# Kernel optimization log

Measured on AMD Instinct MI355X. Metric: run time of the kernel, lower is better.

Reference implementation:

```python
import jax, jax.numpy as jnp
import numpy as np
from jax import lax

B, H, W = 64, 64, 64
N_CHANNELS = 16
N_FILTERS = 128
N_DENSE = 256
T_STEPS = 60  # update_time() with Tmin=60, Tmax=61


def setup_inputs() -> dict:
    key = jax.random.key(0)
    ks = jax.random.split(key, 7)
    s_conv = 1.0 / np.sqrt(3 * 3 * N_CHANNELS)
    s_d1 = 1.0 / np.sqrt(N_FILTERS)
    s_d2 = 1.0 / np.sqrt(N_DENSE)
    return {
        "input": jax.random.uniform(ks[0], (B, H, W), dtype=jnp.float32),
        # conv kernel in HWIO layout for lax.conv_general_dilated
        "conv_w": jax.random.uniform(ks[1], (3, 3, N_CHANNELS, N_FILTERS), jnp.float32, -s_conv, s_conv),
        "conv_b": jax.random.uniform(ks[2], (N_FILTERS,), jnp.float32, -s_conv, s_conv),
        "w1": jax.random.uniform(ks[3], (N_FILTERS, N_DENSE), jnp.float32, -s_d1, s_d1),
        "b1": jax.random.uniform(ks[4], (N_DENSE,), jnp.float32, -s_d1, s_d1),
        "w2": jax.random.uniform(ks[5], (N_DENSE, N_CHANNELS), jnp.float32, -s_d2, s_d2),
        "b2": jax.random.uniform(ks[6], (N_CHANNELS,), jnp.float32, -s_d2, s_d2),
    }


def reference(input, conv_w, conv_b, w1, b1, w2, b2):
    # grid: (B,H,W,C), channel 0 seeded with the input image
    grid = jnp.zeros((B, H, W, N_CHANNELS), dtype=input.dtype)
    grid = grid.at[..., 0].set(input)
    # zero channel 0 of the delta (channel 0 is frozen)
    ch_mask = (jnp.arange(N_CHANNELS) != 0).astype(input.dtype)  # (C,)

    def step(g, _):
        conv = lax.conv_general_dilated(
            g, conv_w, window_strides=(1, 1), padding="SAME",
            dimension_numbers=("NHWC", "HWIO", "NHWC")) + conv_b
        h = jax.nn.relu(conv)                       # (B,H,W,F)
        d = jax.nn.relu(h @ w1 + b1) @ w2 + b2      # (B,H,W,C)
        alive = (g[..., 0:1] > 0.1).astype(g.dtype)  # (B,H,W,1)
        g = g + d * ch_mask * alive
        return g, None

    grid, _ = lax.scan(step, grid, None, length=T_STEPS)
    return jax.nn.softmax(grid[..., 1:11], axis=-1)  # (B,H,W,10)
```

## Files before the change

### kernel.cpp

```cpp
#include <hip/hip_runtime.h>
#include <math.h>

typedef _Float16 f16;
typedef f16  f16x8 __attribute__((ext_vector_type(8)));
typedef f16  f16x4 __attribute__((ext_vector_type(4)));
typedef float f32x4 __attribute__((ext_vector_type(4)));

#define NB 64
#define NC 16
#define NF 128
#define ND 256
#define NSTEP 60
#define GRID_ELEMS (NB*64*64*NC)
#define NPIX (NB*64*64)

#define KCONV 160
#define HSS   136
#define RPS   18

#define OFF_CW 0
#define OFF_W1 20480
#define OFF_W2 53248

__global__ void init_grid(const float* __restrict__ inp, float* __restrict__ g) {
    int i = blockIdx.x * 256 + threadIdx.x;
    if (i >= GRID_ELEMS) return;
    int c = i & 15;
    g[i] = (c == 0) ? inp[i >> 4] : 0.0f;
}

__global__ void prep_weights(const float* __restrict__ cw, const float* __restrict__ w1,
                             const float* __restrict__ w2, f16* __restrict__ wb) {
    int i = blockIdx.x * 256 + threadIdx.x;
    float v; int off, idx;
    if (i < 20480) {
        int f = i / 160, k = i - f * 160;
        v = (k < 144) ? cw[k * 128 + f] : 0.0f;
        off = OFF_CW; idx = i;
    } else if (i < 20480 + 32768) {
        int r = i - 20480;
        int j = r >> 7, f = r & 127;
        v = w1[f * 256 + j];
        off = OFF_W1; idx = r;
    } else {
        int r = i - 20480 - 32768;
        int c = r >> 8, j = r & 255;
        v = w2[j * 16 + c];
        off = OFF_W2; idx = r;
    }
    wb[off + idx] = (f16)v;
}

__global__ __launch_bounds__(256, 2) void nca_step(
    const float* __restrict__ gin, float* __restrict__ gout,
    const f16* __restrict__ wb,
    const float* __restrict__ cb, const float* __restrict__ b1, const float* __restrict__ b2)
{
    __shared__ f16 smem[40000];
    f16* const hs   = smem;
    f16* const halo = smem + 34816;
    float* const redF = (float*)smem;

    const int t    = threadIdx.x;
    const int w    = t >> 6;
    const int lane = t & 63;
    const int q    = lane >> 4;
    const int l16  = lane & 15;

    const int d  = blockIdx.x;
    const int b  = ((d & 7) << 3) | (d >> 7);
    const int tl = (d >> 3) & 15;
    const int y0 = (tl >> 2) << 4;
    const int x0 = (tl & 3) << 4;

    const float* gb  = gin  + (size_t)b * 64 * 64 * 16;
    float*       gob = gout + (size_t)b * 64 * 64 * 16;

    const int fbase = w << 5;
    f16x8 cA[2][5];
    #pragma unroll
    for (int ft = 0; ft < 2; ++ft)
        #pragma unroll
        for (int kc = 0; kc < 5; ++kc)
            cA[ft][kc] = *(const f16x8*)(wb + OFF_CW +
                (size_t)(fbase + ft * 16 + l16) * KCONV + kc * 32 + q * 8);

    for (int i = t; i < 1296; i += 256) {
        int c4 = (i & 3) << 2;
        int xy = i >> 2;
        int xx = xy % 18;
        int yy = xy / 18;
        int gy = y0 + yy - 1, gx = x0 + xx - 1;
        f32x4 v = {0.f, 0.f, 0.f, 0.f};
        if ((unsigned)gy < 64u && (unsigned)gx < 64u)
            v = *(const f32x4*)(gb + (gy * 64 + gx) * 16 + c4);
        f16x4 hv;
        hv.x = (f16)v.x; hv.y = (f16)v.y; hv.z = (f16)v.z; hv.w = (f16)v.w;
        *(f16x4*)(halo + xy * 16 + c4) = hv;
    }
    __syncthreads();

    for (int half = 0; half < 2; ++half) {
        f32x4 acc[2][8];
        #pragma unroll
        for (int ft = 0; ft < 2; ++ft) {
            f32x4 bias;
            bias.x = cb[fbase + ft * 16 + q * 4 + 0];
            bias.y = cb[fbase + ft * 16 + q * 4 + 1];
            bias.z = cb[fbase + ft * 16 + q * 4 + 2];
            bias.w = cb[fbase + ft * 16 + q * 4 + 3];
            #pragma unroll
            for (int p = 0; p < 8; ++p) acc[ft][p] = bias;
        }

        #pragma unroll
        for (int kc = 0; kc < 5; ++kc) {
            int tap = kc * 2 + (q >> 1);
            if (tap > 8) tap = 8;
            int dy = tap / 3, dx = tap - dy * 3;
            #pragma unroll
            for (int p = 0; p < 8; ++p) {
                int hy = half * 8 + p + dy;
                int hx = l16 + dx;
                f16x8 bf = *(const f16x8*)(halo + (hy * 18 + hx) * 16 + (q & 1) * 8);
                #pragma unroll
                for (int ft = 0; ft < 2; ++ft)
                    acc[ft][p] = __builtin_amdgcn_mfma_f32_16x16x32_f16(cA[ft][kc], bf, acc[ft][p], 0, 0, 0);
            }
        }

        #pragma unroll
        for (int ft = 0; ft < 2; ++ft)
            #pragma unroll
            for (int p = 0; p < 8; ++p) {
                f32x4 a = acc[ft][p];
                f16x4 pk;
                pk.x = (f16)fmaxf(a.x, 0.0f);
                pk.y = (f16)fmaxf(a.y, 0.0f);
                pk.z = (f16)fmaxf(a.z, 0.0f);
                pk.w = (f16)fmaxf(a.w, 0.0f);
                *(f16x4*)(hs + (half * 128 + p * 16 + l16) * HSS + fbase + ft * 16 + q * 4) = pk;
            }
    }
    __syncthreads();

    const int tyy = t >> 4, txx = t & 15;
    const size_t tpixb = ((size_t)(y0 + tyy) * 64 + (x0 + txx)) * 16;
    const float a0 = gb[tpixb];
    f32x4 gv4[4];
    #pragma unroll
    for (int h = 0; h < 4; ++h) gv4[h] = *(const f32x4*)(gb + tpixb + h * 4);

    const int jbase = w << 6;
    f16x8 dA[2][2][4];
    float b1v[2][2][4];
    #pragma unroll
    for (int jp = 0; jp < 2; ++jp)
        #pragma unroll
        for (int jt2 = 0; jt2 < 2; ++jt2) {
            #pragma unroll
            for (int kc = 0; kc < 4; ++kc)
                dA[jp][jt2][kc] = *(const f16x8*)(wb + OFF_W1 +
                    (size_t)(jbase + jp * 32 + jt2 * 16 + l16) * 128 + kc * 32 + q * 8);
            #pragma unroll
            for (int r = 0; r < 4; ++r)
                b1v[jp][jt2][r] = b1[jbase + jp * 32 + jt2 * 16 + q * 4 + r];
        }
    f16x4 w2k[4];
    #pragma unroll
    for (int jt = 0; jt < 4; ++jt)
        w2k[jt] = *(const f16x4*)(wb + OFF_W2 + (size_t)l16 * 256 + jbase + jt * 16 + q * 4);

    f32x4 dacc[16];
    #pragma unroll
    for (int p = 0; p < 16; ++p) { dacc[p].x = 0.f; dacc[p].y = 0.f; dacc[p].z = 0.f; dacc[p].w = 0.f; }

    for (int p = 0; p < 16; ++p) {
        f16x8 hB[4];
        #pragma unroll
        for (int kc = 0; kc < 4; ++kc)
            hB[kc] = *(const f16x8*)(hs + (p * 16 + l16) * HSS + kc * 32 + q * 8);

        #pragma unroll
        for (int jp = 0; jp < 2; ++jp)
            #pragma unroll
            for (int jt2 = 0; jt2 < 2; ++jt2) {
                f32x4 a1;
                a1.x = b1v[jp][jt2][0]; a1.y = b1v[jp][jt2][1];
                a1.z = b1v[jp][jt2][2]; a1.w = b1v[jp][jt2][3];
                #pragma unroll
                for (int kc = 0; kc < 4; ++kc)
                    a1 = __builtin_amdgcn_mfma_f32_16x16x32_f16(dA[jp][jt2][kc], hB[kc], a1, 0, 0, 0);
                f16x4 pk;
                pk.x = (f16)fmaxf(a1.x, 0.0f);
                pk.y = (f16)fmaxf(a1.y, 0.0f);
                pk.z = (f16)fmaxf(a1.z, 0.0f);
                pk.w = (f16)fmaxf(a1.w, 0.0f);
                dacc[p] = __builtin_amdgcn_mfma_f32_16x16x16f16(pk, w2k[jp * 2 + jt2], dacc[p], 0, 0, 0);
            }
    }

    __syncthreads();
    #pragma unroll
    for (int p = 0; p < 16; ++p)
        #pragma unroll
        for (int r = 0; r < 4; ++r) {
            int px = p * 16 + q * 4 + r;
            redF[(w * 256 + px) * RPS + l16] = dacc[p][r];
        }
    __syncthreads();

    {
        const int px = t;
        const bool alive = (a0 > 0.1f);
        #pragma unroll
        for (int h = 0; h < 4; ++h) {
            const int ch = h * 4;
            f32x4 v0 = *(const f32x4*)(redF + (0 * 256 + px) * RPS + ch);
            f32x4 v1 = *(const f32x4*)(redF + (1 * 256 + px) * RPS + ch);
            f32x4 v2 = *(const f32x4*)(redF + (2 * 256 + px) * RPS + ch);
            f32x4 v3 = *(const f32x4*)(redF + (3 * 256 + px) * RPS + ch);
            f32x4 sv = v0 + v1 + v2 + v3;
            f32x4 ov;
            #pragma unroll
            for (int i = 0; i < 4; ++i) {
                int c = ch + i;
                float nv = gv4[h][i];
                if (alive && c != 0) nv += sv[i] + b2[c];
                ov[i] = nv;
            }
            *(f32x4*)(gob + tpixb + ch) = ov;
        }
    }
}

__global__ void softmax_out(const float* __restrict__ g, float* __restrict__ out) {
    int pix = blockIdx.x * 256 + threadIdx.x;
    if (pix >= NPIX) return;
    const float* gp = g + (size_t)pix * 16;
    float v[10];
    float m = -1e30f;
    #pragma unroll
    for (int i = 0; i < 10; ++i) { v[i] = gp[1 + i]; m = fmaxf(m, v[i]); }
    float s = 0.f;
    #pragma unroll
    for (int i = 0; i < 10; ++i) { v[i] = __expf(v[i] - m); s += v[i]; }
    float inv = 1.0f / s;
    float* op = out + (size_t)pix * 10;
    #pragma unroll
    for (int i = 0; i < 10; ++i) op[i] = v[i] * inv;
}

extern "C" void kernel_launch(void* const* d_in, const int* in_sizes, int n_in,
                              void* d_out, int out_size, void* d_ws, size_t ws_size,
                              hipStream_t stream) {
    const float* inp = (const float*)d_in[0];
    const float* cw  = (const float*)d_in[1];
    const float* cb  = (const float*)d_in[2];
    const float* w1  = (const float*)d_in[3];
    const float* b1  = (const float*)d_in[4];
    const float* w2  = (const float*)d_in[5];
    const float* b2  = (const float*)d_in[6];
    float* out = (float*)d_out;

    float* g0 = (float*)d_ws;
    float* g1 = g0 + GRID_ELEMS;
    f16* wb = (f16*)d_out;

    prep_weights<<<224, 256, 0, stream>>>(cw, w1, w2, wb);
    init_grid<<<(GRID_ELEMS + 255) / 256, 256, 0, stream>>>(inp, g0);

    float* bufs[2] = { g0, g1 };
    for (int s = 0; s < NSTEP; ++s) {
        nca_step<<<1024, 256, 0, stream>>>(bufs[s & 1], bufs[(s + 1) & 1],
                                           wb, cb, b1, b2);
    }
    softmax_out<<<(NPIX + 255) / 256, 256, 0, stream>>>(g0, out);
}
```

Measured before the change: 2.499 ms.

## Partition dense MLP by pixel rows per wave instead of hidden units, drop LDS reduction

Each wave now owns 4 pixel rows of the tile and loops over all 256 hidden units, keeping the h activations in registers and streaming W1/W2 slices from global memory. Because every wave computes the full sum for its own pixels, the cross-wave LDS reduction and its two barriers are gone, and results are written straight to the output grid. In exchange, weights are reloaded from global/L2 on every hidden tile, not held in registers, and the output stores become scalar per-lane writes instead of vectorised ones.

```diff
diff --git a/kernel.cpp b/kernel.cpp
--- a/kernel.cpp
+++ b/kernel.cpp
@@ -16,7 +16,6 @@
 
 #define KCONV 160
 #define HSS   136
-#define RPS   18
 
 #define OFF_CW 0
 #define OFF_W1 20480
@@ -59,7 +58,6 @@
     __shared__ f16 smem[40000];
     f16* const hs   = smem;
     f16* const halo = smem + 34816;
-    float* const redF = (float*)smem;
 
     const int t    = threadIdx.x;
     const int w    = t >> 6;
@@ -144,92 +142,57 @@
     }
     __syncthreads();
 
-    const int tyy = t >> 4, txx = t & 15;
-    const size_t tpixb = ((size_t)(y0 + tyy) * 64 + (x0 + txx)) * 16;
-    const float a0 = gb[tpixb];
-    f32x4 gv4[4];
-    #pragma unroll
-    for (int h = 0; h < 4; ++h) gv4[h] = *(const f32x4*)(gb + tpixb + h * 4);
-
-    const int jbase = w << 6;
-    f16x8 dA[2][2][4];
-    float b1v[2][2][4];
-    #pragma unroll
-    for (int jp = 0; jp < 2; ++jp)
-        #pragma unroll
-        for (int jt2 = 0; jt2 < 2; ++jt2) {
+    const int pbase = w << 2;
+
+    f16x8 hB[4][4];
+    #pragma unroll
+    for (int pp = 0; pp < 4; ++pp)
+        #pragma unroll
+        for (int kc = 0; kc < 4; ++kc)
+            hB[pp][kc] = *(const f16x8*)(hs + ((pbase + pp) * 16 + l16) * HSS + kc * 32 + q * 8);
+
+    f32x4 dacc[4];
+    #pragma unroll
+    for (int pp = 0; pp < 4; ++pp) { dacc[pp].x = 0.f; dacc[pp].y = 0.f; dacc[pp].z = 0.f; dacc[pp].w = 0.f; }
+
+    #pragma unroll 1
+    for (int jt = 0; jt < 16; ++jt) {
+        f16x8 dAk[4];
+        #pragma unroll
+        for (int kc = 0; kc < 4; ++kc)
+            dAk[kc] = *(const f16x8*)(wb + OFF_W1 +
+                (size_t)(jt * 16 + l16) * 128 + kc * 32 + q * 8);
+        f32x4 b1v = *(const f32x4*)(b1 + jt * 16 + q * 4);
+        f16x4 w2f = *(const f16x4*)(wb + OFF_W2 + (size_t)l16 * 256 + jt * 16 + q * 4);
+
+        #pragma unroll
+        for (int pp = 0; pp < 4; ++pp) {
+            f32x4 a1 = b1v;
             #pragma unroll
             for (int kc = 0; kc < 4; ++kc)
-                dA[jp][jt2][kc] = *(const f16x8*)(wb + OFF_W1 +
-                    (size_t)(jbase + jp * 32 + jt2 * 16 + l16) * 128 + kc * 32 + q * 8);
-            #pragma unroll
-            for (int r = 0; r < 4; ++r)
-                b1v[jp][jt2][r] = b1[jbase + jp * 32 + jt2 * 16 + q * 4 + r];
-        }
-    f16x4 w2k[4];
-    #pragma unroll
-    for (int jt = 0; jt < 4; ++jt)
-        w2k[jt] = *(const f16x4*)(wb + OFF_W2 + (size_t)l16 * 256 + jbase + jt * 16 + q * 4);
-
-    f32x4 dacc[16];
-    #pragma unroll
-    for (int p = 0; p < 16; ++p) { dacc[p].x = 0.f; dacc[p].y = 0.f; dacc[p].z = 0.f; dacc[p].w = 0.f; }
-
-    for (int p = 0; p < 16; ++p) {
-        f16x8 hB[4];
-        #pragma unroll
-        for (int kc = 0; kc < 4; ++kc)
-            hB[kc] = *(const f16x8*)(hs + (p * 16 + l16) * HSS + kc * 32 + q * 8);
-
-        #pragma unroll
-        for (int jp = 0; jp < 2; ++jp)
-            #pragma unroll
-            for (int jt2 = 0; jt2 < 2; ++jt2) {
-                f32x4 a1;
-                a1.x = b1v[jp][jt2][0]; a1.y = b1v[jp][jt2][1];
-                a1.z = b1v[jp][jt2][2]; a1.w = b1v[jp][jt2][3];
-                #pragma unroll
-                for (int kc = 0; kc < 4; ++kc)
-                    a1 = __builtin_amdgcn_mfma_f32_16x16x32_f16(dA[jp][jt2][kc], hB[kc], a1, 0, 0, 0);
-                f16x4 pk;
-                pk.x = (f16)fmaxf(a1.x, 0.0f);
-                pk.y = (f16)fmaxf(a1.y, 0.0f);
-                pk.z = (f16)fmaxf(a1.z, 0.0f);
-                pk.w = (f16)fmaxf(a1.w, 0.0f);
-                dacc[p] = __builtin_amdgcn_mfma_f32_16x16x16f16(pk, w2k[jp * 2 + jt2], dacc[p], 0, 0, 0);
-            }
-    }
-
-    __syncthreads();
-    #pragma unroll
-    for (int p = 0; p < 16; ++p)
+                a1 = __builtin_amdgcn_mfma_f32_16x16x32_f16(dAk[kc], hB[pp][kc], a1, 0, 0, 0);
+            f16x4 pk;
+            pk.x = (f16)fmaxf(a1.x, 0.0f);
+            pk.y = (f16)fmaxf(a1.y, 0.0f);
+            pk.z = (f16)fmaxf(a1.z, 0.0f);
+            pk.w = (f16)fmaxf(a1.w, 0.0f);
+            dacc[pp] = __builtin_amdgcn_mfma_f32_16x16x16f16(pk, w2f, dacc[pp], 0, 0, 0);
+        }
+    }
+
+    const float b2v = b2[l16];
+    #pragma unroll
+    for (int pp = 0; pp < 4; ++pp) {
+        const int prow = pbase + pp;
         #pragma unroll
         for (int r = 0; r < 4; ++r) {
-            int px = p * 16 + q * 4 + r;
-            redF[(w * 256 + px) * RPS + l16] = dacc[p][r];
-        }
-    __syncthreads();
-
-    {
-        const int px = t;
-        const bool alive = (a0 > 0.1f);
-        #pragma unroll
-        for (int h = 0; h < 4; ++h) {
-            const int ch = h * 4;
-            f32x4 v0 = *(const f32x4*)(redF + (0 * 256 + px) * RPS + ch);
-            f32x4 v1 = *(const f32x4*)(redF + (1 * 256 + px) * RPS + ch);
-            f32x4 v2 = *(const f32x4*)(redF + (2 * 256 + px) * RPS + ch);
-            f32x4 v3 = *(const f32x4*)(redF + (3 * 256 + px) * RPS + ch);
-            f32x4 sv = v0 + v1 + v2 + v3;
-            f32x4 ov;
-            #pragma unroll
-            for (int i = 0; i < 4; ++i) {
-                int c = ch + i;
-                float nv = gv4[h][i];
-                if (alive && c != 0) nv += sv[i] + b2[c];
-                ov[i] = nv;
-            }
-            *(f32x4*)(gob + tpixb + ch) = ov;
+            const int px = prow * 16 + q * 4 + r;
+            const int yy = px >> 4, xx = px & 15;
+            const size_t pixb = ((size_t)(y0 + yy) * 64 + (x0 + xx)) * 16;
+            const float a0 = gb[pixb];
+            float nv = gb[pixb + l16];
+            if (a0 > 0.1f && l16 != 0) nv += dacc[pp][r] + b2v;
+            gob[pixb + l16] = nv;
         }
     }
 }
```

New measurement: 3.166 ms. 1.27x slower.

## Repartition waves 2x2 over pixels and filters, stream weights per k-chunk

Applied to the files above, without the earlier changes.

Changes the wave split from four waves each owning a slice of filters and dense units across all 256 pixels to a 2x2 split over pixel halves and filter/dense halves. Conv weights and W1 tiles are now streamed per k-chunk or j-tile with a one-step register prefetch instead of being held entirely in registers. The final cross-wave reduction drops from four partials to two, with the reduction buffer stride changed to 17. The aim is lower register pressure and less reduction traffic, at the cost of more global/L2 weight loads inside the loops and scalar rather than vector LDS reads in the reduction.

```diff
diff --git a/kernel.cpp b/kernel.cpp
--- a/kernel.cpp
+++ b/kernel.cpp
@@ -16,7 +16,7 @@
 
 #define KCONV 160
 #define HSS   136
-#define RPS   18
+#define RPS   17
 
 #define OFF_CW 0
 #define OFF_W1 20480
@@ -67,6 +67,10 @@
     const int q    = lane >> 4;
     const int l16  = lane & 15;
 
+    const int wp = w & 1;
+    const int wf = w >> 1;
+    const int wj = w >> 1;
+
     const int d  = blockIdx.x;
     const int b  = ((d & 7) << 3) | (d >> 7);
     const int tl = (d >> 3) & 15;
@@ -76,14 +80,14 @@
     const float* gb  = gin  + (size_t)b * 64 * 64 * 16;
     float*       gob = gout + (size_t)b * 64 * 64 * 16;
 
-    const int fbase = w << 5;
-    f16x8 cA[2][5];
-    #pragma unroll
-    for (int ft = 0; ft < 2; ++ft)
-        #pragma unroll
-        for (int kc = 0; kc < 5; ++kc)
-            cA[ft][kc] = *(const f16x8*)(wb + OFF_CW +
-                (size_t)(fbase + ft * 16 + l16) * KCONV + kc * 32 + q * 8);
+    const int fbase = wf << 6;
+    const int jbase = wj << 7;
+
+    f16x8 cAc[4], cAn[4];
+    #pragma unroll
+    for (int ft = 0; ft < 4; ++ft)
+        cAc[ft] = *(const f16x8*)(wb + OFF_CW +
+            (size_t)(fbase + ft * 16 + l16) * KCONV + q * 8);
 
     for (int i = t; i < 1296; i += 256) {
         int c4 = (i & 3) << 2;
@@ -100,10 +104,10 @@
     }
     __syncthreads();
 
-    for (int half = 0; half < 2; ++half) {
-        f32x4 acc[2][8];
-        #pragma unroll
-        for (int ft = 0; ft < 2; ++ft) {
+    {
+        f32x4 acc[4][8];
+        #pragma unroll
+        for (int ft = 0; ft < 4; ++ft) {
             f32x4 bias;
             bias.x = cb[fbase + ft * 16 + q * 4 + 0];
             bias.y = cb[fbase + ft * 16 + q * 4 + 1];
@@ -113,24 +117,31 @@
             for (int p = 0; p < 8; ++p) acc[ft][p] = bias;
         }
 
-        #pragma unroll
+        #pragma unroll 1
         for (int kc = 0; kc < 5; ++kc) {
+            int kcn = (kc < 4) ? kc + 1 : 4;
+            #pragma unroll
+            for (int ft = 0; ft < 4; ++ft)
+                cAn[ft] = *(const f16x8*)(wb + OFF_CW +
+                    (size_t)(fbase + ft * 16 + l16) * KCONV + kcn * 32 + q * 8);
             int tap = kc * 2 + (q >> 1);
             if (tap > 8) tap = 8;
             int dy = tap / 3, dx = tap - dy * 3;
             #pragma unroll
             for (int p = 0; p < 8; ++p) {
-                int hy = half * 8 + p + dy;
+                int hy = wp * 8 + p + dy;
                 int hx = l16 + dx;
                 f16x8 bf = *(const f16x8*)(halo + (hy * 18 + hx) * 16 + (q & 1) * 8);
                 #pragma unroll
-                for (int ft = 0; ft < 2; ++ft)
-                    acc[ft][p] = __builtin_amdgcn_mfma_f32_16x16x32_f16(cA[ft][kc], bf, acc[ft][p], 0, 0, 0);
-            }
-        }
-
-        #pragma unroll
-        for (int ft = 0; ft < 2; ++ft)
+                for (int ft = 0; ft < 4; ++ft)
+                    acc[ft][p] = __builtin_amdgcn_mfma_f32_16x16x32_f16(cAc[ft], bf, acc[ft][p], 0, 0, 0);
+            }
+            #pragma unroll
+            for (int ft = 0; ft < 4; ++ft) cAc[ft] = cAn[ft];
+        }
+
+        #pragma unroll
+        for (int ft = 0; ft < 4; ++ft)
             #pragma unroll
             for (int p = 0; p < 8; ++p) {
                 f32x4 a = acc[ft][p];
@@ -139,74 +150,73 @@
                 pk.y = (f16)fmaxf(a.y, 0.0f);
                 pk.z = (f16)fmaxf(a.z, 0.0f);
                 pk.w = (f16)fmaxf(a.w, 0.0f);
-                *(f16x4*)(hs + (half * 128 + p * 16 + l16) * HSS + fbase + ft * 16 + q * 4) = pk;
-            }
-    }
-    __syncthreads();
-
-    const int tyy = t >> 4, txx = t & 15;
-    const size_t tpixb = ((size_t)(y0 + tyy) * 64 + (x0 + txx)) * 16;
+                *(f16x4*)(hs + ((wp * 8 + p) * 16 + l16) * HSS + fbase + ft * 16 + q * 4) = pk;
+            }
+    }
+    __syncthreads();
+
+    const size_t tpixb = ((size_t)(y0 + (t >> 4)) * 64 + (x0 + (t & 15))) * 16;
     const float a0 = gb[tpixb];
     f32x4 gv4[4];
     #pragma unroll
     for (int h = 0; h < 4; ++h) gv4[h] = *(const f32x4*)(gb + tpixb + h * 4);
 
-    const int jbase = w << 6;
-    f16x8 dA[2][2][4];
-    float b1v[2][2][4];
-    #pragma unroll
-    for (int jp = 0; jp < 2; ++jp)
-        #pragma unroll
-        for (int jt2 = 0; jt2 < 2; ++jt2) {
+    f32x4 dacc[8];
+    #pragma unroll
+    for (int p = 0; p < 8; ++p) { dacc[p].x = 0.f; dacc[p].y = 0.f; dacc[p].z = 0.f; dacc[p].w = 0.f; }
+
+    #pragma unroll 1
+    for (int pass = 0; pass < 2; ++pass) {
+        f16x8 hB[4][4];
+        #pragma unroll
+        for (int pp = 0; pp < 4; ++pp)
             #pragma unroll
             for (int kc = 0; kc < 4; ++kc)
-                dA[jp][jt2][kc] = *(const f16x8*)(wb + OFF_W1 +
-                    (size_t)(jbase + jp * 32 + jt2 * 16 + l16) * 128 + kc * 32 + q * 8);
-            #pragma unroll
-            for (int r = 0; r < 4; ++r)
-                b1v[jp][jt2][r] = b1[jbase + jp * 32 + jt2 * 16 + q * 4 + r];
-        }
-    f16x4 w2k[4];
-    #pragma unroll
-    for (int jt = 0; jt < 4; ++jt)
-        w2k[jt] = *(const f16x4*)(wb + OFF_W2 + (size_t)l16 * 256 + jbase + jt * 16 + q * 4);
-
-    f32x4 dacc[16];
-    #pragma unroll
-    for (int p = 0; p < 16; ++p) { dacc[p].x = 0.f; dacc[p].y = 0.f; dacc[p].z = 0.f; dacc[p].w = 0.f; }
-
-    for (int p = 0; p < 16; ++p) {
-        f16x8 hB[4];
+                hB[pp][kc] = *(const f16x8*)(hs +
+                    ((wp * 8 + pass * 4 + pp) * 16 + l16) * HSS + kc * 32 + q * 8);
+
+        f16x8 dAc[4], dAn[4];
         #pragma unroll
         for (int kc = 0; kc < 4; ++kc)
-            hB[kc] = *(const f16x8*)(hs + (p * 16 + l16) * HSS + kc * 32 + q * 8);
-
-        #pragma unroll
-        for (int jp = 0; jp < 2; ++jp)
-            #pragma unroll
-            for (int jt2 = 0; jt2 < 2; ++jt2) {
-                f32x4 a1;
-                a1.x = b1v[jp][jt2][0]; a1.y = b1v[jp][jt2][1];
-                a1.z = b1v[jp][jt2][2]; a1.w = b1v[jp][jt2][3];
+            dAc[kc] = *(const f16x8*)(wb + OFF_W1 +
+                (size_t)(jbase + l16) * 128 + kc * 32 + q * 8);
+
+        #pragma unroll 1
+        for (int jt = 0; jt < 8; ++jt) {
+            int jn = (jt < 7) ? jt + 1 : 7;
+            #pragma unroll
+            for (int kc = 0; kc < 4; ++kc)
+                dAn[kc] = *(const f16x8*)(wb + OFF_W1 +
+                    (size_t)(jbase + jn * 16 + l16) * 128 + kc * 32 + q * 8);
+            f32x4 b1v = *(const f32x4*)(b1 + jbase + jt * 16 + q * 4);
+            f16x4 w2f = *(const f16x4*)(wb + OFF_W2 +
+                (size_t)l16 * 256 + jbase + jt * 16 + q * 4);
+
+            #pragma unroll
+            for (int pp = 0; pp < 4; ++pp) {
+                f32x4 a1 = b1v;
                 #pragma unroll
                 for (int kc = 0; kc < 4; ++kc)
-                    a1 = __builtin_amdgcn_mfma_f32_16x16x32_f16(dA[jp][jt2][kc], hB[kc], a1, 0, 0, 0);
+                    a1 = __builtin_amdgcn_mfma_f32_16x16x32_f16(dAc[kc], hB[pp][kc], a1, 0, 0, 0);
                 f16x4 pk;
                 pk.x = (f16)fmaxf(a1.x, 0.0f);
                 pk.y = (f16)fmaxf(a1.y, 0.0f);
                 pk.z = (f16)fmaxf(a1.z, 0.0f);
                 pk.w = (f16)fmaxf(a1.w, 0.0f);
-                dacc[p] = __builtin_amdgcn_mfma_f32_16x16x16f16(pk, w2k[jp * 2 + jt2], dacc[p], 0, 0, 0);
-            }
-    }
-
-    __syncthreads();
-    #pragma unroll
-    for (int p = 0; p < 16; ++p)
+                dacc[pass * 4 + pp] = __builtin_amdgcn_mfma_f32_16x16x16f16(pk, w2f, dacc[pass * 4 + pp], 0, 0, 0);
+            }
+            #pragma unroll
+            for (int kc = 0; kc < 4; ++kc) dAc[kc] = dAn[kc];
+        }
+    }
+
+    __syncthreads();
+    #pragma unroll
+    for (int p = 0; p < 8; ++p)
         #pragma unroll
         for (int r = 0; r < 4; ++r) {
-            int px = p * 16 + q * 4 + r;
-            redF[(w * 256 + px) * RPS + l16] = dacc[p][r];
+            int px = (wp * 8 + p) * 16 + q * 4 + r;
+            redF[(wj * 256 + px) * RPS + l16] = dacc[p][r];
         }
     __syncthreads();
 
@@ -216,17 +226,14 @@
         #pragma unroll
         for (int h = 0; h < 4; ++h) {
             const int ch = h * 4;
-            f32x4 v0 = *(const f32x4*)(redF + (0 * 256 + px) * RPS + ch);
-            f32x4 v1 = *(const f32x4*)(redF + (1 * 256 + px) * RPS + ch);
-            f32x4 v2 = *(const f32x4*)(redF + (2 * 256 + px) * RPS + ch);
-            f32x4 v3 = *(const f32x4*)(redF + (3 * 256 + px) * RPS + ch);
-            f32x4 sv = v0 + v1 + v2 + v3;
             f32x4 ov;
             #pragma unroll
             for (int i = 0; i < 4; ++i) {
                 int c = ch + i;
+                float sv = redF[(0 * 256 + px) * RPS + c]
+                         + redF[(1 * 256 + px) * RPS + c];
                 float nv = gv4[h][i];
-                if (alive && c != 0) nv += sv[i] + b2[c];
+                if (alive && c != 0) nv += sv + b2[c];
                 ov[i] = nv;
             }
             *(f32x4*)(gob + tpixb + ch) = ov;
```

Measured after the change: 4.231 ms. 1.69x slower.

## Replace per-step kernel launches with a persistent kernel and grid barrier

Applied to the files above, without the earlier changes.

The 60 per-step kernel launches are replaced by one persistent kernel of 512 blocks. Each block processes two tiles per step and then waits at a two-level atomic grid barrier (group counters feeding a root counter), with the counters stored in the output buffer and zeroed by prep_weights. This is meant to remove launch overhead and the tail drain between steps. In exchange it depends on all 512 blocks being co-resident (two per CU under the launch bounds), adds spin-wait cost, and has a guard counter that could break out of the wait early.

```diff
diff --git a/kernel.cpp b/kernel.cpp
--- a/kernel.cpp
+++ b/kernel.cpp
@@ -21,6 +21,7 @@
 #define OFF_CW 0
 #define OFF_W1 20480
 #define OFF_W2 53248
+#define BAR_OFF_F16 65536
 
 __global__ void init_grid(const float* __restrict__ inp, float* __restrict__ g) {
     int i = blockIdx.x * 256 + threadIdx.x;
@@ -32,6 +33,10 @@
 __global__ void prep_weights(const float* __restrict__ cw, const float* __restrict__ w1,
                              const float* __restrict__ w2, f16* __restrict__ wb) {
     int i = blockIdx.x * 256 + threadIdx.x;
+    if (blockIdx.x == 0) {
+        unsigned* barp = (unsigned*)(wb + BAR_OFF_F16);
+        for (int z = threadIdx.x; z < 320; z += 256) barp[z] = 0u;
+    }
     float v; int off, idx;
     if (i < 20480) {
         int f = i / 160, k = i - f * 160;
@@ -51,12 +56,12 @@
     wb[off + idx] = (f16)v;
 }
 
-__global__ __launch_bounds__(256, 2) void nca_step(
-    const float* __restrict__ gin, float* __restrict__ gout,
+__device__ __forceinline__ void process_tile(
+    int d, const float* __restrict__ gin, float* __restrict__ gout,
     const f16* __restrict__ wb,
-    const float* __restrict__ cb, const float* __restrict__ b1, const float* __restrict__ b2)
+    const float* __restrict__ cb, const float* __restrict__ b1, const float* __restrict__ b2,
+    f16* smem)
 {
-    __shared__ f16 smem[40000];
     f16* const hs   = smem;
     f16* const halo = smem + 34816;
     float* const redF = (float*)smem;
@@ -67,7 +72,6 @@
     const int q    = lane >> 4;
     const int l16  = lane & 15;
 
-    const int d  = blockIdx.x;
     const int b  = ((d & 7) << 3) | (d >> 7);
     const int tl = (d >> 3) & 15;
     const int y0 = (tl >> 2) << 4;
@@ -232,6 +236,52 @@
             *(f32x4*)(gob + tpixb + ch) = ov;
         }
     }
+    __syncthreads();
+}
+
+__global__ __launch_bounds__(256, 2) void nca_persist(
+    float* g0, float* g1, const f16* __restrict__ wb,
+    const float* __restrict__ cb, const float* __restrict__ b1, const float* __restrict__ b2,
+    unsigned* bar)
+{
+    __shared__ f16 smem[40000];
+    const int dd  = blockIdx.x;
+    const int grp = dd & 7;
+    unsigned* root = bar;
+    unsigned* cx   = bar + 32 + (grp << 5);
+
+    unsigned r0 = 0, x0 = 0;
+    if (threadIdx.x == 0) {
+        r0 = __hip_atomic_load(root, __ATOMIC_RELAXED, __HIP_MEMORY_SCOPE_AGENT);
+        x0 = __hip_atomic_load(cx,   __ATOMIC_RELAXED, __HIP_MEMORY_SCOPE_AGENT);
+    }
+
+    for (int s = 0; s < NSTEP; ++s) {
+        const float* gin = (s & 1) ? g1 : g0;
+        float*       gout = (s & 1) ? g0 : g1;
+
+        #pragma unroll 1
+        for (int ti = 0; ti < 2; ++ti)
+            process_tile(dd + ti * 512, gin, gout, wb, cb, b1, b2, smem);
+
+        if (s < NSTEP - 1) {
+            __syncthreads();
+            if (threadIdx.x == 0) {
+                __threadfence();
+                unsigned old = atomicAdd(cx, 1u);
+                if (((old - x0) & 63u) == 63u)
+                    atomicAdd(root, 1u);
+                const unsigned need = (unsigned)(s + 1) * 8u;
+                int guard = 0;
+                while (__hip_atomic_load(root, __ATOMIC_RELAXED, __HIP_MEMORY_SCOPE_AGENT) - r0 < need) {
+                    __builtin_amdgcn_s_sleep(8);
+                    if (++guard > 10000000) break;
+                }
+                __threadfence();
+            }
+            __syncthreads();
+        }
+    }
 }
 
 __global__ void softmax_out(const float* __restrict__ g, float* __restrict__ out) {
@@ -266,14 +316,12 @@
     float* g0 = (float*)d_ws;
     float* g1 = g0 + GRID_ELEMS;
     f16* wb = (f16*)d_out;
+    unsigned* bar = (unsigned*)((char*)d_out + 131072);
 
     prep_weights<<<224, 256, 0, stream>>>(cw, w1, w2, wb);
     init_grid<<<(GRID_ELEMS + 255) / 256, 256, 0, stream>>>(inp, g0);
 
-    float* bufs[2] = { g0, g1 };
-    for (int s = 0; s < NSTEP; ++s) {
-        nca_step<<<1024, 256, 0, stream>>>(bufs[s & 1], bufs[(s + 1) & 1],
-                                           wb, cb, b1, b2);
-    }
+    nca_persist<<<512, 256, 0, stream>>>(g0, g1, wb, cb, b1, b2, bar);
+
     softmax_out<<<(NPIX + 255) / 256, 256, 0, stream>>>(g0, out);
 }
```

Result: slower. 3.352 ms (+34.1%).
